# Optimization experiments

Measured on AMD Instinct MI355X. Metric: run time of the kernel, lower is better.

Reference implementation:

```python
import jax, jax.numpy as jnp
import numpy as np

N_ATOMS = 20
N_IN, N_EMB_N, N_EMB_E, N_H_N, N_H_E = 4, 128, 128, 256, 256


def lstm_seq(x, Wi, bi, Wh, bh):
    """x: [B, M, T, D] -> h sequence [B, M, T, H]. Gates stacked as (i,f,g,o).
    Equivalent to the per-gate nn.Linear pairs: bi/bh are the two bias vectors."""
    B, M, T, D = x.shape
    H = Wh.shape[0]
    # precompute all input-to-hidden projections in one big GEMM: [T,B,M,4H]
    xg = jnp.einsum('bmtd,dg->tbmg', x, Wi) + bi

    def step(carry, xg_t):
        c, h = carry
        g = xg_t + h @ Wh + bh  # [B,M,4H]
        i, f, gg, o = jnp.split(g, 4, axis=-1)
        i = jax.nn.sigmoid(i)
        f = jax.nn.sigmoid(f)
        gg = jnp.tanh(gg)
        o = jax.nn.sigmoid(o)
        c = f * c + i * gg
        h = o * jnp.tanh(c)
        return (c, h), h

    z = jnp.zeros((B, M, H), x.dtype)
    _, hs = jax.lax.scan(step, (z, z), xg)  # hs: [T,B,M,H]
    return jnp.transpose(hs, (1, 2, 0, 3))


def setup_inputs() -> dict:
    key = jax.random.key(0)
    ks = jax.random.split(key, 16)
    s = 0.05
    # fully-connected directed edges without self loops -> one-hot incidence
    send, rec = np.where(~np.eye(N_ATOMS, dtype=bool))
    eye = np.eye(N_ATOMS, dtype=np.float32)
    inp = {
        'X': jax.random.normal(ks[0], (16, N_ATOMS, 64, N_IN), jnp.float32),
        'rel_rec': jnp.asarray(eye[rec]),
        'rel_send': jnp.asarray(eye[send]),
        # motion embedding fc
        'Wm': jax.random.normal(ks[1], (N_IN, N_EMB_N), jnp.float32) * s,
        'bm': jnp.zeros((N_EMB_N,), jnp.float32),
        # motion LSTM (gates i,f,g,o stacked)
        'Wmi': jax.random.normal(ks[2], (N_EMB_N, 4 * N_H_N), jnp.float32) * s,
        'bmi': jnp.zeros((4 * N_H_N,), jnp.float32),
        'Wmh': jax.random.normal(ks[3], (N_H_N, 4 * N_H_N), jnp.float32) * s,
        'bmh': jnp.zeros((4 * N_H_N,), jnp.float32),
        # interaction embedding fc (in = 2*n_h_node)
        'We': jax.random.normal(ks[4], (2 * N_H_N, N_EMB_E), jnp.float32) * s,
        'be': jnp.zeros((N_EMB_E,), jnp.float32),
        # edge LSTM
        'Wei': jax.random.normal(ks[5], (N_EMB_E, 4 * N_H_E), jnp.float32) * s,
        'bei': jnp.zeros((4 * N_H_E,), jnp.float32),
        'Weh': jax.random.normal(ks[6], (N_H_E, 4 * N_H_E), jnp.float32) * s,
        'beh': jnp.zeros((4 * N_H_E,), jnp.float32),
        # output fc
        'Wf': jax.random.normal(ks[7], (N_H_E, 1), jnp.float32) * s,
        'bf': jnp.zeros((1,), jnp.float32),
    }
    return inp


def reference(X, rel_rec, rel_send, Wm, bm, Wmi, bmi, Wmh, bmh,
              We, be, Wei, bei, Weh, beh, Wf, bf):
    # Motion embedding on temporal deltas: [B,N,T-1,n_emb_node]
    dX = X[:, :, 1:, :] - X[:, :, :-1, :]
    em = dX @ Wm + bm
    # Motion LSTM, full sequence: [B,N,T-1,Hn]
    hm = lstm_seq(em, Wmi, bmi, Wmh, bmh)
    # Interaction embedding: gather per-edge sender/receiver node states
    senders = jnp.einsum('en,bnth->beth', rel_send, hm)
    receivers = jnp.einsum('en,bnth->beth', rel_rec, hm)
    edges = jnp.concatenate([senders, receivers], axis=-1)  # [B,E,T-1,2Hn]
    ea = edges @ We + be  # [B,E,T-1,n_emb_edge]
    # Edge LSTM, last hidden state: [B,E,He]
    he = lstm_seq(ea, Wei, bei, Weh, beh)[:, :, -1, :]
    # Edge scores -> dense adjacency via incidence matrices
    A = jax.nn.sigmoid(he @ Wf + bf)[..., 0]  # [B,E]
    Ad = jnp.einsum('en,be,em->bnm', rel_send, A, rel_rec)  # send^T diag(A) rec
    return 0.5 * (Ad + jnp.transpose(Ad, (0, 2, 1)))  # symmetrize
```

## Files before the change

kernel.cpp:

```cpp
#include <hip/hip_runtime.h>
#include <stdint.h>

#define NBATCH 16
#define NNODE  20
#define TSTEPS 63
#define NEDGE  380
#define HID    256
#define RS     280

typedef __bf16 bf16x8 __attribute__((ext_vector_type(8)));
typedef float  f32x4  __attribute__((ext_vector_type(4)));

__device__ __forceinline__ float bf2f(unsigned short u){
  union { unsigned int i; float f; } v; v.i = ((unsigned int)u) << 16; return v.f;
}
__device__ __forceinline__ unsigned short f2bf(float f){
  union { float f; unsigned int i; } v; v.f = f;
  return (unsigned short)((v.i + 0x7FFFu + ((v.i >> 16) & 1u)) >> 16);
}
__device__ __forceinline__ bf16x8 as_frag(uint4 v){
  union { uint4 u; bf16x8 b; } c; c.u = v; return c.b;
}
__device__ __forceinline__ float sigmf(float x){ return 1.0f/(1.0f+__expf(-x)); }
__device__ __forceinline__ float tanh_f(float x){ float e=__expf(2.0f*x); return (e-1.0f)/(e+1.0f); }

__device__ __forceinline__ unsigned long long load_ax(const unsigned long long* p){
  return __hip_atomic_load(p, __ATOMIC_RELAXED, __HIP_MEMORY_SCOPE_AGENT);
}
__device__ __forceinline__ void store_ax(unsigned long long* p, unsigned long long v){
  __hip_atomic_store(p, v, __ATOMIC_RELAXED, __HIP_MEMORY_SCOPE_AGENT);
}
__device__ __forceinline__ void wait_vm0(){ asm volatile("s_waitcnt vmcnt(0)" ::: "memory"); }

__device__ __forceinline__ void xpose4(f32x4& v, int cl){
  float s0 = __shfl_xor((float)v[1], 1), s1 = __shfl_xor((float)v[0], 1);
  float s2 = __shfl_xor((float)v[3], 1), s3 = __shfl_xor((float)v[2], 1);
  bool b0 = (cl & 1);
  float a0 = b0 ? s0 : v[0], a1 = b0 ? v[1] : s1;
  float a2 = b0 ? s2 : v[2], a3 = b0 ? v[3] : s3;
  float t0 = __shfl_xor(a2, 2), t1 = __shfl_xor(a3, 2);
  float t2 = __shfl_xor(a0, 2), t3 = __shfl_xor(a1, 2);
  bool b1 = (cl & 2);
  v[0] = b1 ? t0 : a0; v[1] = b1 ? t1 : a1;
  v[2] = b1 ? a2 : t2; v[3] = b1 ? a3 : t3;
}

__global__ __launch_bounds__(256) void prep_a(
    const float* __restrict__ We, const float* __restrict__ Wei,
    const float* __restrict__ Wm, const float* __restrict__ Wmi,
    const float* __restrict__ bm, const float* __restrict__ bmi, const float* __restrict__ bmh,
    const float* __restrict__ be, const float* __restrict__ bei, const float* __restrict__ beh,
    float* __restrict__ Wse, float* __restrict__ Wre, float* __restrict__ WcmGI,
    float* __restrict__ bcmGI, float* __restrict__ bceGI,
    float* __restrict__ Afin, unsigned int* __restrict__ ectr, unsigned int* __restrict__ mctr){
  int bid = blockIdx.x, tid = threadIdx.x;
  if (bid < 2048){
    int idx = bid*256 + tid;
    int half = idx >> 18;
    int j = idx & 262143;
    int k = j >> 10, nn = j & 1023;
    const float* Wrow = We + (half*256 + k)*128;
    float s = 0.f;
    for (int d = 0; d < 128; ++d) s += Wrow[d] * Wei[d*1024 + nn];
    (half ? Wre : Wse)[k*1024 + nn] = s;
  } else if (bid < 2064){
    int idx = (bid-2048)*256 + tid;
    int d = idx >> 10, ci = idx & 1023;
    int col = (ci & 3)*256 + (ci >> 2);
    float s = 0.f;
    for (int j = 0; j < 128; ++j) s += Wm[d*128 + j] * Wmi[j*1024 + col];
    WcmGI[idx] = s;
  } else if (bid < 2068){
    int ci = (bid-2064)*256 + tid;
    int col = (ci & 3)*256 + (ci >> 2);
    float s = bmi[col] + bmh[col];
    for (int j = 0; j < 128; ++j) s += bm[j] * Wmi[j*1024 + col];
    bcmGI[ci] = s;
  } else if (bid < 2072){
    int ci = (bid-2068)*256 + tid;
    int col = (ci & 3)*256 + (ci >> 2);
    float s = bei[col] + beh[col];
    for (int j = 0; j < 128; ++j) s += be[j] * Wei[j*1024 + col];
    bceGI[ci] = s;
  } else if (bid == 2072){
    for (int i = tid; i < 2048; i += 256) ectr[i] = 0u;
    for (int i = tid; i < 1024; i += 256) mctr[i] = 0u;
  } else {
    int idx = (bid-2073)*256 + tid;
    if (idx < NBATCH*NEDGE) Afin[idx] = 0.f;
  }
}

__device__ __forceinline__ void pack_gi(const float* __restrict__ W,
                                        unsigned short* __restrict__ dst, int id){
  int lane = id & 63, kt = (id >> 6) & 7, tt = (id >> 9) & 1, w = (id >> 10) & 7, nb = id >> 13;
  int cl = lane & 15, q = lane >> 4;
  int gcol = (cl & 3)*256 + nb*64 + (w*2 + tt)*4 + (cl >> 2);
  int k0 = kt*32 + q*8;
  unsigned int wb[4];
  #pragma unroll
  for (int p = 0; p < 4; ++p){
    unsigned short a = f2bf(W[(k0+2*p  )*1024 + gcol]);
    unsigned short b = f2bf(W[(k0+2*p+1)*1024 + gcol]);
    wb[p] = (unsigned int)a | ((unsigned int)b << 16);
  }
  ((uint4*)dst)[id] = make_uint4(wb[0], wb[1], wb[2], wb[3]);
}

__device__ __forceinline__ void pack_one(const float* __restrict__ S,
                                         unsigned short* __restrict__ dst, int id, int n){
  int lane = id & 63, kt = (id >> 6) & 7;
  int k0 = kt*32 + ((lane >> 4) << 3);
  unsigned int wb[4];
  #pragma unroll
  for (int p = 0; p < 4; ++p){
    unsigned short a = f2bf(S[(k0+2*p  )*1024 + n]);
    unsigned short b = f2bf(S[(k0+2*p+1)*1024 + n]);
    wb[p] = (unsigned int)a | ((unsigned int)b << 16);
  }
  ((uint4*)dst)[id] = make_uint4(wb[0], wb[1], wb[2], wb[3]);
}

__global__ __launch_bounds__(256) void prep_b(
    const float* __restrict__ Wmh, const float* __restrict__ Weh,
    const float* __restrict__ Wse, const float* __restrict__ Wre,
    unsigned short* __restrict__ pWmh, unsigned short* __restrict__ pWeh,
    unsigned short* __restrict__ pWsr){
  int gid = blockIdx.x*256 + threadIdx.x;
  if (gid < 32768){
    pack_gi(Wmh, pWmh, gid);
  } else if (gid < 65536){
    pack_gi(Weh, pWeh, gid - 32768);
  } else {
    int id = gid - 65536;
    int ng = (id >> 9)*16 + (id & 15);
    const float* S = (ng < 1024) ? Wse : Wre;
    pack_one(S, pWsr, id, ng & 1023);
  }
}

__global__ __launch_bounds__(512, 2) void motion_lstm(
    const float* __restrict__ X, const float* __restrict__ WcmGI,
    const float* __restrict__ bcmGI, const unsigned short* __restrict__ pWmh,
    unsigned short* __restrict__ hm, unsigned short* __restrict__ mb,
    unsigned int* __restrict__ mctr){
  __shared__ __align__(16) unsigned short hst[16*RS];
  __shared__ float dxs[10*252];
  __shared__ __align__(16) float sWc[4*256];
  __shared__ __align__(16) float sbc[256];
  int tid = threadIdx.x, lane = tid & 63, w = tid >> 6;
  int l15 = lane & 15, quad = lane >> 4;
  int m = blockIdx.x & 31, n = blockIdx.x >> 5;
  int s0 = m*10;
  unsigned int* ctr = mctr + m*32;

  uint4 wreg[2][8];
  #pragma unroll
  for (int tt = 0; tt < 2; ++tt)
    #pragma unroll
    for (int kt = 0; kt < 8; ++kt)
      wreg[tt][kt] = ((const uint4*)pWmh)[(((n*8 + w)*2 + tt)*8 + kt)*64 + lane];

  uint4 z4 = make_uint4(0,0,0,0);
  for (int i = tid; i < 560; i += 512) ((uint4*)hst)[i] = z4;
  for (int i = tid; i < 1024; i += 512) sWc[i] = WcmGI[(i >> 8)*1024 + n*256 + (i & 255)];
  if (tid < 256) sbc[tid] = bcmGI[n*256 + tid];
  for (int i = tid; i < 2520; i += 512){
    int sl = i / 252; int r = i % 252; int t = r >> 2; int d = r & 3;
    const float* Xp = X + (((size_t)(s0 + sl)*64 + t)*4 + d);
    dxs[i] = Xp[4] - Xp[0];
  }
  __syncthreads();

  float bb[2] = { sbc[(w*2+0)*16 + l15], sbc[(w*2+1)*16 + l15] };
  int row = quad*4 + (l15 & 3);
  int hsub = l15 >> 2;
  int slr = row < 10 ? row : 9;
  float ce[2] = {0.f, 0.f};

  for (int t = 0; t < TSTEPS; ++t){
    if (t > 0){
      if (tid == 0){
        unsigned int tgt = 4u*(unsigned)t;
        while (__hip_atomic_load(ctr, __ATOMIC_RELAXED, __HIP_MEMORY_SCOPE_AGENT) < tgt)
          __builtin_amdgcn_s_sleep(1);
      }
      __syncthreads();
      const unsigned long long* mbp = (const unsigned long long*)mb
          + ((size_t)((t-1)&1)*32 + m)*16*64;
      unsigned long long pv[2]; int po[2] = {-1,-1};
      #pragma unroll
      for (int j = 0; j < 2; ++j){
        int i = tid + j*512;
        if (i < 768){
          int which = i >> 8, jj = i & 255;
          int r = jj >> 4, c = jj & 15;
          int np = which + (which >= n ? 1 : 0);
          pv[j] = load_ax(&mbp[(size_t)r*64 + np*16 + c]);
          po[j] = r*RS + np*64 + c*4;
        }
      }
      #pragma unroll
      for (int j = 0; j < 2; ++j)
        if (po[j] >= 0) *(unsigned long long*)&hst[po[j]] = pv[j];
    }
    __syncthreads();

    f32x4 acc[2];
    acc[0] = (f32x4){bb[0],bb[0],bb[0],bb[0]};
    acc[1] = (f32x4){bb[1],bb[1],bb[1],bb[1]};
    #pragma unroll
    for (int kt = 0; kt < 8; ++kt){
      bf16x8 a = as_frag(*(const uint4*)&hst[l15*RS + kt*32 + quad*8]);
      acc[0] = __builtin_amdgcn_mfma_f32_16x16x32_bf16(a, as_frag(wreg[0][kt]), acc[0], 0, 0, 0);
      acc[1] = __builtin_amdgcn_mfma_f32_16x16x32_bf16(a, as_frag(wreg[1][kt]), acc[1], 0, 0, 0);
    }
    __syncthreads();

    f32x4 dxv = *(const f32x4*)&dxs[slr*252 + t*4];
    #pragma unroll
    for (int tt = 0; tt < 2; ++tt){
      int tl = w*2 + tt;
      f32x4 v = acc[tt];
      xpose4(v, l15);
      #pragma unroll
      for (int d = 0; d < 4; ++d){
        f32x4 wv = *(const f32x4*)&sWc[d*256 + tl*16 + hsub*4];
        v[0] += dxv[d]*wv[0]; v[1] += dxv[d]*wv[1];
        v[2] += dxv[d]*wv[2]; v[3] += dxv[d]*wv[3];
      }
      float iv = sigmf(v[0]), fv = sigmf(v[1]), gg = tanh_f(v[2]), ov = sigmf(v[3]);
      float cc = fv*ce[tt] + iv*gg; ce[tt] = cc;
      hst[row*RS + n*64 + tl*4 + hsub] = f2bf(ov*tanh_f(cc));
    }
    __syncthreads();

    unsigned long long* mbc = (unsigned long long*)mb
        + ((size_t)(t&1)*32 + m)*16*64;
    if (tid < 256){
      int r = tid >> 4, c = tid & 15;
      unsigned long long v = *(const unsigned long long*)&hst[r*RS + n*64 + c*4];
      if (t < 62) store_ax(&mbc[(size_t)r*64 + n*16 + c], v);
      if (r < 10){
        int seq = s0 + r;
        int b2 = seq / 20, nd = seq - (seq/20)*20;
        *(unsigned long long*)&hm[(((size_t)(b2*63 + t)*20) + nd)*256 + n*64 + c*4] = v;
      }
    }
    wait_vm0();
    __syncthreads();
    if (t < 62 && tid == 0)
      __hip_atomic_fetch_add(ctr, 1u, __ATOMIC_RELAXED, __HIP_MEMORY_SCOPE_AGENT);
  }
}

__global__ __launch_bounds__(256) void gsr_gemm(
    const unsigned short* __restrict__ hm, const unsigned short* __restrict__ pWsr,
    unsigned short* __restrict__ gsrT){
  __shared__ __align__(16) unsigned short scol[128*100];
  int tid = threadIdx.x, lane = tid & 63, wid = tid >> 6;
  int l15 = lane & 15, quad = lane >> 4;
  int bm = blockIdx.x % 252, bn = blockIdx.x / 252;
  int rowbase = bm*80;
  f32x4 acc[5][2] = {};
  #pragma unroll
  for (int kt = 0; kt < 8; ++kt){
    bf16x8 af[5];
    #pragma unroll
    for (int mt = 0; mt < 5; ++mt)
      af[mt] = as_frag(*(const uint4*)&hm[(size_t)(rowbase + mt*16 + l15)*256 + kt*32 + quad*8]);
    #pragma unroll
    for (int j = 0; j < 2; ++j){
      int ntg = bn*8 + wid*2 + j;
      bf16x8 bfr = as_frag(*(const uint4*)&pWsr[(((size_t)ntg*8 + kt)*64 + lane)*8]);
      #pragma unroll
      for (int mt = 0; mt < 5; ++mt)
        acc[mt][j] = __builtin_amdgcn_mfma_f32_16x16x32_bf16(af[mt], bfr, acc[mt][j], 0, 0, 0);
    }
  }
  #pragma unroll
  for (int mt = 0; mt < 5; ++mt)
    #pragma unroll
    for (int j = 0; j < 2; ++j){
      int colL = (wid*2 + j)*16 + l15;
      unsigned int p0 = (unsigned)f2bf(acc[mt][j][0]) | ((unsigned)f2bf(acc[mt][j][1]) << 16);
      unsigned int p1 = (unsigned)f2bf(acc[mt][j][2]) | ((unsigned)f2bf(acc[mt][j][3]) << 16);
      *(uint2*)&scol[colL*100 + mt*16 + quad*4] = make_uint2(p0, p1);
    }
  __syncthreads();
  int half = bn >> 3;
  #pragma unroll
  for (int rep = 0; rep < 2; ++rep){
    int i = tid + rep*256;
    int btl = i >> 7, colL = i & 127;
    const unsigned short* sp = &scol[colL*100 + btl*20];
    uint2 u0 = *(const uint2*)(sp);
    uint2 u1 = *(const uint2*)(sp+4);
    uint2 u2 = *(const uint2*)(sp+8);
    uint2 u3 = *(const uint2*)(sp+12);
    uint2 u4 = *(const uint2*)(sp+16);
    unsigned short* dp = gsrT + ((size_t)(bm*4 + btl)*1024 + (bn&7)*128 + colL)*48;
    if (half){
      *(uint4*)(dp)      = make_uint4(u0.x, u0.y, u1.x, u1.y);
      *(uint4*)(dp + 8)  = make_uint4(u2.x, u2.y, u3.x, u3.y);
      *(uint2*)(dp + 16) = u4;
    } else {
      unsigned int o0 = u0.x, o1 = u0.y, o2 = u1.x & 0xffffu;
      unsigned int o3 = (u1.x >> 16) | (u1.y << 16);
      unsigned int o4 = (u1.y >> 16) | (u2.x << 16);
      unsigned int o5 = u2.x >> 16;
      unsigned int o6 = u2.y, o7 = u3.x, o8 = u3.y & 0xffffu;
      unsigned int o9 = (u3.y >> 16) | (u4.x << 16);
      unsigned int o10 = (u4.x >> 16) | (u4.y << 16);
      unsigned int o11 = u4.y >> 16;
      *(uint4*)(dp + 24) = make_uint4(o0, o1, o2, o3);
      *(uint4*)(dp + 32) = make_uint4(o4, o5, o6, o7);
      *(uint4*)(dp + 40) = make_uint4(o8, o9, o10, o11);
    }
  }
}

__device__ __forceinline__ void stage_gxb(const unsigned short* __restrict__ gsrT,
                                          unsigned short* __restrict__ gx,
                                          int tid, int b, int m, int n, int tq){
  const unsigned short* base = gsrT + (size_t)(b*63 + tq)*1024*48;
  int c = tid >> 1, chv = tid & 1;
  int g = c >> 6, hh = c & 63;
  const unsigned short* src = base + (size_t)((g << 8) + (n << 6) + hh)*48;
  unsigned short* dst = gx + (hh >> 2)*640 + (((hh & 3) << 2) + g)*40;
  if (chv == 0){
    *(uint4*)(dst)      = *(const uint4*)(src);
    *(uint4*)(dst + 8)  = *(const uint4*)(src + 8);
    *(uint2*)(dst + 16) = *(const uint2*)(src + 16);
  } else {
    const unsigned int* s3 = (const unsigned int*)(src + 24 + 6*m);
    unsigned int* d3 = (unsigned int*)(dst + 24);
    d3[0] = s3[0]; d3[1] = s3[1]; d3[2] = s3[2];
  }
}

__global__ __launch_bounds__(512, 2) void edge_lstm(
    const unsigned short* __restrict__ gsrT, const float* __restrict__ bceGI,
    const unsigned short* __restrict__ pWeh, const float* __restrict__ Wf,
    unsigned short* __restrict__ hb, float* __restrict__ Afin,
    unsigned int* __restrict__ ectr){
  __shared__ __align__(16) unsigned short hst[96*RS];
  __shared__ __align__(16) unsigned short gxb[2][10240];
  __shared__ __align__(16) float sbce[256];
  __shared__ __align__(16) float sWf[64];
  int tid = threadIdx.x, lane = tid & 63, w = tid >> 6;
  int l15 = lane & 15, quad = lane >> 4;
  int bid = blockIdx.x;
  int n = bid >> 6, G = bid & 63, b = G >> 2, m = G & 3;
  int e0 = m*95;
  unsigned int* ctr = ectr + G*32;

  uint4 wreg[2][8];
  #pragma unroll
  for (int tt = 0; tt < 2; ++tt)
    #pragma unroll
    for (int kt = 0; kt < 8; ++kt)
      wreg[tt][kt] = ((const uint4*)pWeh)[(((n*8 + w)*2 + tt)*8 + kt)*64 + lane];

  uint4 aoh[6];
  #pragma unroll
  for (int mt = 0; mt < 6; ++mt){
    int row = mt*16 + l15;
    int e = e0 + (row < 95 ? row : 94);
    int s = e / 19; int rr = e - s*19;
    int sr = s - m*5;
    int rc = rr + (rr >= s ? 1 : 0);
    unsigned int wd[4];
    #pragma unroll
    for (int p = 0; p < 4; ++p){
      int k0 = quad*8 + 2*p, k1 = k0 + 1;
      unsigned short a0 = ((k0 < 20) ? (rc == k0) : (k0 >= 24 && k0 < 29 && sr == k0-24)) ? 0x3F80 : 0;
      unsigned short a1 = ((k1 < 20) ? (rc == k1) : (k1 >= 24 && k1 < 29 && sr == k1-24)) ? 0x3F80 : 0;
      wd[p] = (unsigned int)a0 | ((unsigned int)a1 << 16);
    }
    aoh[mt] = make_uint4(wd[0], wd[1], wd[2], wd[3]);
  }

  if (tid < 256) sbce[tid] = bceGI[n*256 + tid];
  if (tid < 64)  sWf[tid]  = Wf[n*64 + tid];
  uint4 z4 = make_uint4(0,0,0,0);
  for (int i = tid; i < 3360; i += 512) ((uint4*)hst)[i] = z4;
  for (int i = tid; i < 2560; i += 512) ((uint4*)gxb)[i] = z4;
  __syncthreads();
  stage_gxb(gsrT, &gxb[0][0], tid, b, m, n, 0);
  __syncthreads();

  float bb[2]  = { sbce[(w*2+0)*16 + l15], sbce[(w*2+1)*16 + l15] };
  float wfr[2] = { sWf[(w*2+0)*4 + (l15>>2)], sWf[(w*2+1)*4 + (l15>>2)] };

  float ce[2][6]; float epi[6];
  #pragma unroll
  for (int mt = 0; mt < 6; ++mt){ ce[0][mt] = 0.f; ce[1][mt] = 0.f; epi[mt] = 0.f; }

  for (int t = 0; t < TSTEPS; ++t){
    int par = t & 1, nxt = par ^ 1;
    if (t > 0){
      if (tid == 0){
        unsigned int tgt = 4u*(unsigned)t;
        while (__hip_atomic_load(ctr, __ATOMIC_RELAXED, __HIP_MEMORY_SCOPE_AGENT) < tgt)
          __builtin_amdgcn_s_sleep(1);
      }
      __syncthreads();
      const unsigned long long* hbp = (const unsigned long long*)hb
          + (((size_t)((t-1)&1)*16 + b)*4 + m)*96*64;
      unsigned long long pv[9]; int po[9];
      #pragma unroll
      for (int j = 0; j < 9; ++j){
        int i = tid + j*512;
        int which = i / 1536, jj = i - which*1536;
        int r = jj >> 4, c = jj & 15;
        int np = which + (which >= n ? 1 : 0);
        pv[j] = load_ax(&hbp[(size_t)r*64 + np*16 + c]);
        po[j] = r*RS + np*64 + c*4;
      }
      #pragma unroll
      for (int j = 0; j < 9; ++j)
        *(unsigned long long*)&hst[po[j]] = pv[j];
    }
    if (t + 1 < TSTEPS)
      stage_gxb(gsrT, &gxb[nxt][0], tid, b, m, n, t+1);
    __syncthreads();

    f32x4 acc[2][6];
    #pragma unroll
    for (int mt = 0; mt < 6; ++mt){
      acc[0][mt] = (f32x4){bb[0],bb[0],bb[0],bb[0]};
      acc[1][mt] = (f32x4){bb[1],bb[1],bb[1],bb[1]};
    }
    #pragma unroll
    for (int kt = 0; kt < 8; ++kt){
      bf16x8 a[6];
      #pragma unroll
      for (int mt = 0; mt < 6; ++mt)
        a[mt] = as_frag(*(const uint4*)&hst[(mt*16 + l15)*RS + kt*32 + quad*8]);
      #pragma unroll
      for (int mt = 0; mt < 6; ++mt){
        acc[0][mt] = __builtin_amdgcn_mfma_f32_16x16x32_bf16(a[mt], as_frag(wreg[0][kt]), acc[0][mt], 0, 0, 0);
        acc[1][mt] = __builtin_amdgcn_mfma_f32_16x16x32_bf16(a[mt], as_frag(wreg[1][kt]), acc[1][mt], 0, 0, 0);
      }
    }
    {
      bf16x8 bx0 = as_frag(*(const uint4*)&gxb[par][(w*2+0)*640 + l15*40 + quad*8]);
      bf16x8 bx1 = as_frag(*(const uint4*)&gxb[par][(w*2+1)*640 + l15*40 + quad*8]);
      #pragma unroll
      for (int mt = 0; mt < 6; ++mt){
        acc[0][mt] = __builtin_amdgcn_mfma_f32_16x16x32_bf16(as_frag(aoh[mt]), bx0, acc[0][mt], 0, 0, 0);
        acc[1][mt] = __builtin_amdgcn_mfma_f32_16x16x32_bf16(as_frag(aoh[mt]), bx1, acc[1][mt], 0, 0, 0);
      }
    }
    __syncthreads();

    #pragma unroll
    for (int tt = 0; tt < 2; ++tt){
      int tl = w*2 + tt;
      #pragma unroll
      for (int mt = 0; mt < 6; ++mt){
        f32x4 v = acc[tt][mt];
        xpose4(v, l15);
        float iv = sigmf(v[0]), fv = sigmf(v[1]), gg = tanh_f(v[2]), ov = sigmf(v[3]);
        float cc = fv*ce[tt][mt] + iv*gg; ce[tt][mt] = cc;
        float h = ov*tanh_f(cc);
        if (t < 62){
          int row = mt*16 + quad*4 + (l15 & 3);
          hst[row*RS + n*64 + tl*4 + (l15>>2)] = f2bf(h);
        } else {
          epi[mt] += h * wfr[tt];
        }
      }
    }
    if (t < 62){
      __syncthreads();
      unsigned long long* hbc = (unsigned long long*)hb
          + (((size_t)(t&1)*16 + b)*4 + m)*96*64;
      #pragma unroll
      for (int j = 0; j < 3; ++j){
        int i = tid + j*512;
        int r = i >> 4, c = i & 15;
        unsigned long long v = *(const unsigned long long*)&hst[r*RS + n*64 + c*4];
        store_ax(&hbc[(size_t)r*64 + n*16 + c], v);
      }
      wait_vm0();
      __syncthreads();
      if (tid == 0)
        __hip_atomic_fetch_add(ctr, 1u, __ATOMIC_RELAXED, __HIP_MEMORY_SCOPE_AGENT);
    }
  }
  #pragma unroll
  for (int mt = 0; mt < 6; ++mt){
    float v = epi[mt];
    v += __shfl_xor(v, 4);
    v += __shfl_xor(v, 8);
    if (l15 < 4){
      int row = mt*16 + quad*4 + l15;
      if (row < 95)
        atomicAdd(&Afin[b*380 + e0 + row], v);
    }
  }
}

__global__ __launch_bounds__(256) void finalize(const float* __restrict__ Afin,
                                                const float* __restrict__ bfp,
                                                float* __restrict__ out){
  int idx = blockIdx.x*256 + threadIdx.x;
  if (idx >= 16*400) return;
  int b = idx / 400; int ij = idx % 400; int i = ij / 20; int j = ij % 20;
  float v = 0.f;
  if (i != j){
    int e1 = i*19 + j - (j > i ? 1 : 0);
    int e2 = j*19 + i - (i > j ? 1 : 0);
    float bf = bfp[0];
    v = 0.5f*(sigmf(Afin[b*380 + e1] + bf) + sigmf(Afin[b*380 + e2] + bf));
  }
  out[idx] = v;
}

extern "C" void kernel_launch(void* const* d_in, const int* in_sizes, int n_in,
                              void* d_out, int out_size, void* d_ws, size_t ws_size,
                              hipStream_t stream){
  (void)in_sizes; (void)n_in; (void)out_size; (void)ws_size;
  const float* X   = (const float*)d_in[0];
  const float* Wm  = (const float*)d_in[3];
  const float* bm  = (const float*)d_in[4];
  const float* Wmi = (const float*)d_in[5];
  const float* bmi = (const float*)d_in[6];
  const float* Wmh = (const float*)d_in[7];
  const float* bmh = (const float*)d_in[8];
  const float* We  = (const float*)d_in[9];
  const float* be  = (const float*)d_in[10];
  const float* Wei = (const float*)d_in[11];
  const float* bei = (const float*)d_in[12];
  const float* Weh = (const float*)d_in[13];
  const float* beh = (const float*)d_in[14];
  const float* Wf  = (const float*)d_in[15];
  const float* bfp = (const float*)d_in[16];

  char* ws = (char*)d_ws;
  float* Wse   = (float*)(ws + 0);
  float* Wre   = (float*)(ws + 1048576);
  float* WcmGI = (float*)(ws + 2097152);
  float* bcmGI = (float*)(ws + 2113536);
  float* bceGI = (float*)(ws + 2117632);
  unsigned short* pWmh = (unsigned short*)(ws + 2121728);
  unsigned short* pWeh = (unsigned short*)(ws + 2646016);
  unsigned short* pWsr = (unsigned short*)(ws + 3170304);
  unsigned short* hm   = (unsigned short*)(ws + 4218880);
  unsigned short* gsrT = (unsigned short*)(ws + 14540800);
  unsigned short* hb   = (unsigned short*)(ws + 113631232);
  unsigned short* mb   = hb;
  float* Afin          = (float*)(ws + 119922688);
  unsigned int* ectr   = (unsigned int*)(ws + 119947264);
  unsigned int* mctr   = (unsigned int*)(ws + 119955456);
  float* out = (float*)d_out;

  hipLaunchKernelGGL(prep_a, dim3(2097), dim3(256), 0, stream,
                     We, Wei, Wm, Wmi, bm, bmi, bmh, be, bei, beh,
                     Wse, Wre, WcmGI, bcmGI, bceGI, Afin, ectr, mctr);
  hipLaunchKernelGGL(prep_b, dim3(512), dim3(256), 0, stream,
                     Wmh, Weh, Wse, Wre, pWmh, pWeh, pWsr);
  {
    void* margs[] = {(void*)&X, (void*)&WcmGI, (void*)&bcmGI, (void*)&pWmh,
                     (void*)&hm, (void*)&mb, (void*)&mctr};
    hipLaunchCooperativeKernel(reinterpret_cast<void*>(motion_lstm),
                               dim3(128), dim3(512), margs, 0, stream);
  }
  hipLaunchKernelGGL(gsr_gemm, dim3(252*16), dim3(256), 0, stream,
                     hm, pWsr, gsrT);
  {
    void* eargs[] = {(void*)&gsrT, (void*)&bceGI, (void*)&pWeh, (void*)&Wf,
                     (void*)&hb, (void*)&Afin, (void*)&ectr};
    hipLaunchCooperativeKernel(reinterpret_cast<void*>(edge_lstm),
                               dim3(256), dim3(512), eargs, 0, stream);
  }
  hipLaunchKernelGGL(finalize, dim3(25), dim3(256), 0, stream,
                     Afin, bfp, out);
}
```

Measured before the change: 1.055 ms.

## Split edge LSTM over 512 blocks with 48-edge row groups

Re-partitions the cooperative edge LSTM from 256 blocks of 95 edges each to 512 blocks of 48 edges each. The gsr layout now stores the sender projection for every sender, so a block can read four sender rows at an arbitrary offset. Shared hidden-state staging, counters and MFMA tiles shrink to match, and launch bounds rise to allow more blocks per CU. This spreads the serial recurrence across more CUs to cut per-step latency, at the cost of more inter-block synchronisation traffic and partly wasted tiles.

```diff
diff --git a/kernel.cpp b/kernel.cpp
--- a/kernel.cpp
+++ b/kernel.cpp
@@ -83,7 +83,7 @@
     for (int j = 0; j < 128; ++j) s += be[j] * Wei[j*1024 + col];
     bceGI[ci] = s;
   } else if (bid == 2072){
-    for (int i = tid; i < 2048; i += 256) ectr[i] = 0u;
+    for (int i = tid; i < 4096; i += 256) ectr[i] = 0u;
     for (int i = tid; i < 1024; i += 256) mctr[i] = 0u;
   } else {
     int idx = (bid-2073)*256 + tid;
@@ -288,7 +288,8 @@
       *(uint2*)&scol[colL*100 + mt*16 + quad*4] = make_uint2(p0, p1);
     }
   __syncthreads();
-  int half = bn >> 3;
+  int recv = bn >> 3;
+  int doff = recv ? 0 : 24;
   #pragma unroll
   for (int rep = 0; rep < 2; ++rep){
     int i = tid + rep*256;
@@ -299,30 +300,16 @@
     uint2 u2 = *(const uint2*)(sp+8);
     uint2 u3 = *(const uint2*)(sp+12);
     uint2 u4 = *(const uint2*)(sp+16);
-    unsigned short* dp = gsrT + ((size_t)(bm*4 + btl)*1024 + (bn&7)*128 + colL)*48;
-    if (half){
-      *(uint4*)(dp)      = make_uint4(u0.x, u0.y, u1.x, u1.y);
-      *(uint4*)(dp + 8)  = make_uint4(u2.x, u2.y, u3.x, u3.y);
-      *(uint2*)(dp + 16) = u4;
-    } else {
-      unsigned int o0 = u0.x, o1 = u0.y, o2 = u1.x & 0xffffu;
-      unsigned int o3 = (u1.x >> 16) | (u1.y << 16);
-      unsigned int o4 = (u1.y >> 16) | (u2.x << 16);
-      unsigned int o5 = u2.x >> 16;
-      unsigned int o6 = u2.y, o7 = u3.x, o8 = u3.y & 0xffffu;
-      unsigned int o9 = (u3.y >> 16) | (u4.x << 16);
-      unsigned int o10 = (u4.x >> 16) | (u4.y << 16);
-      unsigned int o11 = u4.y >> 16;
-      *(uint4*)(dp + 24) = make_uint4(o0, o1, o2, o3);
-      *(uint4*)(dp + 32) = make_uint4(o4, o5, o6, o7);
-      *(uint4*)(dp + 40) = make_uint4(o8, o9, o10, o11);
-    }
+    unsigned short* dp = gsrT + ((size_t)(bm*4 + btl)*1024 + (bn&7)*128 + colL)*48 + doff;
+    *(uint4*)(dp)      = make_uint4(u0.x, u0.y, u1.x, u1.y);
+    *(uint4*)(dp + 8)  = make_uint4(u2.x, u2.y, u3.x, u3.y);
+    *(uint2*)(dp + 16) = u4;
   }
 }
 
 __device__ __forceinline__ void stage_gxb(const unsigned short* __restrict__ gsrT,
                                           unsigned short* __restrict__ gx,
-                                          int tid, int b, int m, int n, int tq){
+                                          int tid, int b, int smin, int n, int tq){
   const unsigned short* base = gsrT + (size_t)(b*63 + tq)*1024*48;
   int c = tid >> 1, chv = tid & 1;
   int g = c >> 6, hh = c & 63;
@@ -333,26 +320,27 @@
     *(uint4*)(dst + 8)  = *(const uint4*)(src + 8);
     *(uint2*)(dst + 16) = *(const uint2*)(src + 16);
   } else {
-    const unsigned int* s3 = (const unsigned int*)(src + 24 + 6*m);
-    unsigned int* d3 = (unsigned int*)(dst + 24);
-    d3[0] = s3[0]; d3[1] = s3[1]; d3[2] = s3[2];
-  }
-}
-
-__global__ __launch_bounds__(512, 2) void edge_lstm(
+    const unsigned short* s3 = src + 24 + smin;
+    dst[24] = s3[0]; dst[25] = s3[1]; dst[26] = s3[2]; dst[27] = s3[3];
+  }
+}
+
+__global__ __launch_bounds__(512, 4) void edge_lstm(
     const unsigned short* __restrict__ gsrT, const float* __restrict__ bceGI,
     const unsigned short* __restrict__ pWeh, const float* __restrict__ Wf,
     unsigned short* __restrict__ hb, float* __restrict__ Afin,
     unsigned int* __restrict__ ectr){
-  __shared__ __align__(16) unsigned short hst[96*RS];
+  __shared__ __align__(16) unsigned short hst[48*RS];
   __shared__ __align__(16) unsigned short gxb[2][10240];
   __shared__ __align__(16) float sbce[256];
   __shared__ __align__(16) float sWf[64];
   int tid = threadIdx.x, lane = tid & 63, w = tid >> 6;
   int l15 = lane & 15, quad = lane >> 4;
   int bid = blockIdx.x;
-  int n = bid >> 6, G = bid & 63, b = G >> 2, m = G & 3;
-  int e0 = m*95;
+  int n = bid >> 7, G = bid & 127, b = G >> 3, m = G & 7;
+  int e0 = m*48;
+  int valid = NEDGE - e0 < 48 ? NEDGE - e0 : 48;
+  int smin = e0 / 19;
   unsigned int* ctr = ectr + G*32;
 
   uint4 wreg[2][8];
@@ -362,20 +350,20 @@
     for (int kt = 0; kt < 8; ++kt)
       wreg[tt][kt] = ((const uint4*)pWeh)[(((n*8 + w)*2 + tt)*8 + kt)*64 + lane];
 
-  uint4 aoh[6];
-  #pragma unroll
-  for (int mt = 0; mt < 6; ++mt){
+  uint4 aoh[3];
+  #pragma unroll
+  for (int mt = 0; mt < 3; ++mt){
     int row = mt*16 + l15;
-    int e = e0 + (row < 95 ? row : 94);
+    int e = e0 + (row < valid ? row : valid-1);
     int s = e / 19; int rr = e - s*19;
-    int sr = s - m*5;
+    int sr = s - smin;
     int rc = rr + (rr >= s ? 1 : 0);
     unsigned int wd[4];
     #pragma unroll
     for (int p = 0; p < 4; ++p){
       int k0 = quad*8 + 2*p, k1 = k0 + 1;
-      unsigned short a0 = ((k0 < 20) ? (rc == k0) : (k0 >= 24 && k0 < 29 && sr == k0-24)) ? 0x3F80 : 0;
-      unsigned short a1 = ((k1 < 20) ? (rc == k1) : (k1 >= 24 && k1 < 29 && sr == k1-24)) ? 0x3F80 : 0;
+      unsigned short a0 = ((k0 < 20) ? (rc == k0) : (k0 >= 24 && k0 < 28 && sr == k0-24)) ? 0x3F80 : 0;
+      unsigned short a1 = ((k1 < 20) ? (rc == k1) : (k1 >= 24 && k1 < 28 && sr == k1-24)) ? 0x3F80 : 0;
       wd[p] = (unsigned int)a0 | ((unsigned int)a1 << 16);
     }
     aoh[mt] = make_uint4(wd[0], wd[1], wd[2], wd[3]);
@@ -384,18 +372,18 @@
   if (tid < 256) sbce[tid] = bceGI[n*256 + tid];
   if (tid < 64)  sWf[tid]  = Wf[n*64 + tid];
   uint4 z4 = make_uint4(0,0,0,0);
-  for (int i = tid; i < 3360; i += 512) ((uint4*)hst)[i] = z4;
+  for (int i = tid; i < 1680; i += 512) ((uint4*)hst)[i] = z4;
   for (int i = tid; i < 2560; i += 512) ((uint4*)gxb)[i] = z4;
   __syncthreads();
-  stage_gxb(gsrT, &gxb[0][0], tid, b, m, n, 0);
+  stage_gxb(gsrT, &gxb[0][0], tid, b, smin, n, 0);
   __syncthreads();
 
   float bb[2]  = { sbce[(w*2+0)*16 + l15], sbce[(w*2+1)*16 + l15] };
   float wfr[2] = { sWf[(w*2+0)*4 + (l15>>2)], sWf[(w*2+1)*4 + (l15>>2)] };
 
-  float ce[2][6]; float epi[6];
-  #pragma unroll
-  for (int mt = 0; mt < 6; ++mt){ ce[0][mt] = 0.f; ce[1][mt] = 0.f; epi[mt] = 0.f; }
+  float ce[2][3]; float epi[3];
+  #pragma unroll
+  for (int mt = 0; mt < 3; ++mt){ ce[0][mt] = 0.f; ce[1][mt] = 0.f; epi[mt] = 0.f; }
 
   for (int t = 0; t < TSTEPS; ++t){
     int par = t & 1, nxt = par ^ 1;
@@ -407,39 +395,41 @@
       }
       __syncthreads();
       const unsigned long long* hbp = (const unsigned long long*)hb
-          + (((size_t)((t-1)&1)*16 + b)*4 + m)*96*64;
-      unsigned long long pv[9]; int po[9];
-      #pragma unroll
-      for (int j = 0; j < 9; ++j){
+          + (((size_t)((t-1)&1)*16 + b)*8 + m)*48*64;
+      unsigned long long pv[5]; int po[5] = {-1,-1,-1,-1,-1};
+      #pragma unroll
+      for (int j = 0; j < 5; ++j){
         int i = tid + j*512;
-        int which = i / 1536, jj = i - which*1536;
-        int r = jj >> 4, c = jj & 15;
-        int np = which + (which >= n ? 1 : 0);
-        pv[j] = load_ax(&hbp[(size_t)r*64 + np*16 + c]);
-        po[j] = r*RS + np*64 + c*4;
-      }
-      #pragma unroll
-      for (int j = 0; j < 9; ++j)
-        *(unsigned long long*)&hst[po[j]] = pv[j];
+        if (i < 2304){
+          int which = i / 768, jj = i - which*768;
+          int r = jj >> 4, c = jj & 15;
+          int np = which + (which >= n ? 1 : 0);
+          pv[j] = load_ax(&hbp[(size_t)r*64 + np*16 + c]);
+          po[j] = r*RS + np*64 + c*4;
+        }
+      }
+      #pragma unroll
+      for (int j = 0; j < 5; ++j)
+        if (po[j] >= 0) *(unsigned long long*)&hst[po[j]] = pv[j];
     }
     if (t + 1 < TSTEPS)
-      stage_gxb(gsrT, &gxb[nxt][0], tid, b, m, n, t+1);
+      stage_gxb(gsrT, &gxb[nxt][0], tid, b, smin, n, t+1);
     __syncthreads();
 
-    f32x4 acc[2][6];
-    #pragma unroll
-    for (int mt = 0; mt < 6; ++mt){
+    f32x4 acc[2][3];
+    #pragma unroll
+    for (int mt = 0; mt < 3; ++mt){
       acc[0][mt] = (f32x4){bb[0],bb[0],bb[0],bb[0]};
       acc[1][mt] = (f32x4){bb[1],bb[1],bb[1],bb[1]};
     }
     #pragma unroll
     for (int kt = 0; kt < 8; ++kt){
-      bf16x8 a[6];
-      #pragma unroll
-      for (int mt = 0; mt < 6; ++mt)
+      bf16x8 a[3];
+      #pragma unroll
+      for (int mt = 0; mt < 3; ++mt)
         a[mt] = as_frag(*(const uint4*)&hst[(mt*16 + l15)*RS + kt*32 + quad*8]);
       #pragma unroll
-      for (int mt = 0; mt < 6; ++mt){
+      for (int mt = 0; mt < 3; ++mt){
         acc[0][mt] = __builtin_amdgcn_mfma_f32_16x16x32_bf16(a[mt], as_frag(wreg[0][kt]), acc[0][mt], 0, 0, 0);
         acc[1][mt] = __builtin_amdgcn_mfma_f32_16x16x32_bf16(a[mt], as_frag(wreg[1][kt]), acc[1][mt], 0, 0, 0);
       }
@@ -448,7 +438,7 @@
       bf16x8 bx0 = as_frag(*(const uint4*)&gxb[par][(w*2+0)*640 + l15*40 + quad*8]);
       bf16x8 bx1 = as_frag(*(const uint4*)&gxb[par][(w*2+1)*640 + l15*40 + quad*8]);
       #pragma unroll
-      for (int mt = 0; mt < 6; ++mt){
+      for (int mt = 0; mt < 3; ++mt){
         acc[0][mt] = __builtin_amdgcn_mfma_f32_16x16x32_bf16(as_frag(aoh[mt]), bx0, acc[0][mt], 0, 0, 0);
         acc[1][mt] = __builtin_amdgcn_mfma_f32_16x16x32_bf16(as_frag(aoh[mt]), bx1, acc[1][mt], 0, 0, 0);
       }
@@ -459,7 +449,7 @@
     for (int tt = 0; tt < 2; ++tt){
       int tl = w*2 + tt;
       #pragma unroll
-      for (int mt = 0; mt < 6; ++mt){
+      for (int mt = 0; mt < 3; ++mt){
         f32x4 v = acc[tt][mt];
         xpose4(v, l15);
         float iv = sigmf(v[0]), fv = sigmf(v[1]), gg = tanh_f(v[2]), ov = sigmf(v[3]);
@@ -476,13 +466,15 @@
     if (t < 62){
       __syncthreads();
       unsigned long long* hbc = (unsigned long long*)hb
-          + (((size_t)(t&1)*16 + b)*4 + m)*96*64;
-      #pragma unroll
-      for (int j = 0; j < 3; ++j){
+          + (((size_t)(t&1)*16 + b)*8 + m)*48*64;
+      #pragma unroll
+      for (int j = 0; j < 2; ++j){
         int i = tid + j*512;
-        int r = i >> 4, c = i & 15;
-        unsigned long long v = *(const unsigned long long*)&hst[r*RS + n*64 + c*4];
-        store_ax(&hbc[(size_t)r*64 + n*16 + c], v);
+        if (i < 768){
+          int r = i >> 4, c = i & 15;
+          unsigned long long v = *(const unsigned long long*)&hst[r*RS + n*64 + c*4];
+          store_ax(&hbc[(size_t)r*64 + n*16 + c], v);
+        }
       }
       wait_vm0();
       __syncthreads();
@@ -491,13 +483,13 @@
     }
   }
   #pragma unroll
-  for (int mt = 0; mt < 6; ++mt){
+  for (int mt = 0; mt < 3; ++mt){
     float v = epi[mt];
     v += __shfl_xor(v, 4);
     v += __shfl_xor(v, 8);
     if (l15 < 4){
       int row = mt*16 + quad*4 + l15;
-      if (row < 95)
+      if (row < valid)
         atomicAdd(&Afin[b*380 + e0 + row], v);
     }
   }
@@ -554,7 +546,7 @@
   unsigned short* mb   = hb;
   float* Afin          = (float*)(ws + 119922688);
   unsigned int* ectr   = (unsigned int*)(ws + 119947264);
-  unsigned int* mctr   = (unsigned int*)(ws + 119955456);
+  unsigned int* mctr   = (unsigned int*)(ws + 119963648);
   float* out = (float*)d_out;
 
   hipLaunchKernelGGL(prep_a, dim3(2097), dim3(256), 0, stream,
@@ -574,7 +566,7 @@
     void* eargs[] = {(void*)&gsrT, (void*)&bceGI, (void*)&pWeh, (void*)&Wf,
                      (void*)&hb, (void*)&Afin, (void*)&ectr};
     hipLaunchCooperativeKernel(reinterpret_cast<void*>(edge_lstm),
-                               dim3(256), dim3(512), eargs, 0, stream);
+                               dim3(512), dim3(512), eargs, 0, stream);
   }
   hipLaunchKernelGGL(finalize, dim3(25), dim3(256), 0, stream,
                      Afin, bfp, out);
```

Measured after the change: 1.510 ms. +43.1%, slower.

## Double-buffer LSTM hidden state and publish h directly from registers

Applied to the files above, without the earlier changes.

Both recurrent LSTM kernels now keep two hidden-state buffers in shared memory. Each step's new h is written to the next buffer and packed across lanes with shuffles so it can be stored straight to the global exchange buffer and hm. This removes two __syncthreads and the shared-memory read-back pass per timestep. The gsr_gemm output layout is also simplified so both halves use the same contiguous store path, and the staging reads adjust to match. Spin-waits gain an iteration cap, and the counter regions are enlarged and moved.

```diff
diff --git a/kernel.cpp b/kernel.cpp
--- a/kernel.cpp
+++ b/kernel.cpp
@@ -7,6 +7,7 @@
 #define NEDGE  380
 #define HID    256
 #define RS     280
+#define SPIN_MAX (1u << 23)
 
 typedef __bf16 bf16x8 __attribute__((ext_vector_type(8)));
 typedef float  f32x4  __attribute__((ext_vector_type(4)));
@@ -31,6 +32,14 @@
   __hip_atomic_store(p, v, __ATOMIC_RELAXED, __HIP_MEMORY_SCOPE_AGENT);
 }
 __device__ __forceinline__ void wait_vm0(){ asm volatile("s_waitcnt vmcnt(0)" ::: "memory"); }
+
+__device__ __forceinline__ void spin_until(const unsigned int* ctr, unsigned int tgt){
+  unsigned int guard = 0;
+  while (__hip_atomic_load(ctr, __ATOMIC_RELAXED, __HIP_MEMORY_SCOPE_AGENT) < tgt){
+    if (++guard > SPIN_MAX) break;
+    __builtin_amdgcn_s_sleep(1);
+  }
+}
 
 __device__ __forceinline__ void xpose4(f32x4& v, int cl){
   float s0 = __shfl_xor((float)v[1], 1), s1 = __shfl_xor((float)v[0], 1);
@@ -43,6 +52,14 @@
   bool b1 = (cl & 2);
   v[0] = b1 ? t0 : a0; v[1] = b1 ? t1 : a1;
   v[2] = b1 ? a2 : t2; v[3] = b1 ? a3 : t3;
+}
+
+__device__ __forceinline__ unsigned long long pack_h4(unsigned int hv, int l15){
+  unsigned int o4 = (unsigned int)__shfl_xor((int)hv, 4);
+  unsigned int lo = ((l15 & 4) == 0) ? ((hv & 0xffffu) | (o4 << 16))
+                                     : ((o4 & 0xffffu) | (hv << 16));
+  unsigned int hi = (unsigned int)__shfl_xor((int)lo, 8);
+  return ((unsigned long long)hi << 32) | (unsigned long long)lo;
 }
 
 __global__ __launch_bounds__(256) void prep_a(
@@ -83,7 +100,7 @@
     for (int j = 0; j < 128; ++j) s += be[j] * Wei[j*1024 + col];
     bceGI[ci] = s;
   } else if (bid == 2072){
-    for (int i = tid; i < 2048; i += 256) ectr[i] = 0u;
+    for (int i = tid; i < 4096; i += 256) ectr[i] = 0u;
     for (int i = tid; i < 1024; i += 256) mctr[i] = 0u;
   } else {
     int idx = (bid-2073)*256 + tid;
@@ -144,7 +161,7 @@
     const float* __restrict__ bcmGI, const unsigned short* __restrict__ pWmh,
     unsigned short* __restrict__ hm, unsigned short* __restrict__ mb,
     unsigned int* __restrict__ mctr){
-  __shared__ __align__(16) unsigned short hst[16*RS];
+  __shared__ __align__(16) unsigned short hst[2][16*RS];
   __shared__ float dxs[10*252];
   __shared__ __align__(16) float sWc[4*256];
   __shared__ __align__(16) float sbc[256];
@@ -162,7 +179,7 @@
       wreg[tt][kt] = ((const uint4*)pWmh)[(((n*8 + w)*2 + tt)*8 + kt)*64 + lane];
 
   uint4 z4 = make_uint4(0,0,0,0);
-  for (int i = tid; i < 560; i += 512) ((uint4*)hst)[i] = z4;
+  for (int i = tid; i < 1120; i += 512) ((uint4*)hst)[i] = z4;
   for (int i = tid; i < 1024; i += 512) sWc[i] = WcmGI[(i >> 8)*1024 + n*256 + (i & 255)];
   if (tid < 256) sbc[tid] = bcmGI[n*256 + tid];
   for (int i = tid; i < 2520; i += 512){
@@ -179,12 +196,9 @@
   float ce[2] = {0.f, 0.f};
 
   for (int t = 0; t < TSTEPS; ++t){
+    int par = t & 1, nxt = par ^ 1;
     if (t > 0){
-      if (tid == 0){
-        unsigned int tgt = 4u*(unsigned)t;
-        while (__hip_atomic_load(ctr, __ATOMIC_RELAXED, __HIP_MEMORY_SCOPE_AGENT) < tgt)
-          __builtin_amdgcn_s_sleep(1);
-      }
+      if (tid == 0) spin_until(ctr, 4u*(unsigned)t);
       __syncthreads();
       const unsigned long long* mbp = (const unsigned long long*)mb
           + ((size_t)((t-1)&1)*32 + m)*16*64;
@@ -202,7 +216,7 @@
       }
       #pragma unroll
       for (int j = 0; j < 2; ++j)
-        if (po[j] >= 0) *(unsigned long long*)&hst[po[j]] = pv[j];
+        if (po[j] >= 0) *(unsigned long long*)&hst[par][po[j]] = pv[j];
     }
     __syncthreads();
 
@@ -211,12 +225,13 @@
     acc[1] = (f32x4){bb[1],bb[1],bb[1],bb[1]};
     #pragma unroll
     for (int kt = 0; kt < 8; ++kt){
-      bf16x8 a = as_frag(*(const uint4*)&hst[l15*RS + kt*32 + quad*8]);
+      bf16x8 a = as_frag(*(const uint4*)&hst[par][l15*RS + kt*32 + quad*8]);
       acc[0] = __builtin_amdgcn_mfma_f32_16x16x32_bf16(a, as_frag(wreg[0][kt]), acc[0], 0, 0, 0);
       acc[1] = __builtin_amdgcn_mfma_f32_16x16x32_bf16(a, as_frag(wreg[1][kt]), acc[1], 0, 0, 0);
     }
-    __syncthreads();
-
+
+    unsigned long long* mbc = (unsigned long long*)mb
+        + ((size_t)(t&1)*32 + m)*16*64;
     f32x4 dxv = *(const f32x4*)&dxs[slr*252 + t*4];
     #pragma unroll
     for (int tt = 0; tt < 2; ++tt){
@@ -231,26 +246,25 @@
       }
       float iv = sigmf(v[0]), fv = sigmf(v[1]), gg = tanh_f(v[2]), ov = sigmf(v[3]);
       float cc = fv*ce[tt] + iv*gg; ce[tt] = cc;
-      hst[row*RS + n*64 + tl*4 + hsub] = f2bf(ov*tanh_f(cc));
-    }
-    __syncthreads();
-
-    unsigned long long* mbc = (unsigned long long*)mb
-        + ((size_t)(t&1)*32 + m)*16*64;
-    if (tid < 256){
-      int r = tid >> 4, c = tid & 15;
-      unsigned long long v = *(const unsigned long long*)&hst[r*RS + n*64 + c*4];
-      if (t < 62) store_ax(&mbc[(size_t)r*64 + n*16 + c], v);
-      if (r < 10){
-        int seq = s0 + r;
-        int b2 = seq / 20, nd = seq - (seq/20)*20;
-        *(unsigned long long*)&hm[(((size_t)(b2*63 + t)*20) + nd)*256 + n*64 + c*4] = v;
-      }
-    }
-    wait_vm0();
-    __syncthreads();
-    if (t < 62 && tid == 0)
-      __hip_atomic_fetch_add(ctr, 1u, __ATOMIC_RELAXED, __HIP_MEMORY_SCOPE_AGENT);
+      unsigned short hb16 = f2bf(ov*tanh_f(cc));
+      if (t < 62) hst[nxt][row*RS + n*64 + tl*4 + hsub] = hb16;
+      unsigned long long uv = pack_h4((unsigned int)hb16, l15);
+      if ((l15 & 12) == 0){
+        int r = quad*4 + l15;
+        if (t < 62) store_ax(&mbc[(size_t)r*64 + n*16 + w*2 + tt], uv);
+        if (r < 10){
+          int seq = s0 + r;
+          int b2 = seq / 20, nd = seq - b2*20;
+          *(unsigned long long*)&hm[(((size_t)(b2*63 + t)*20) + nd)*256 + n*64 + tl*4] = uv;
+        }
+      }
+    }
+    if (t < 62){
+      wait_vm0();
+      __syncthreads();
+      if (tid == 0)
+        __hip_atomic_fetch_add(ctr, 1u, __ATOMIC_RELAXED, __HIP_MEMORY_SCOPE_AGENT);
+    }
   }
 }
 
@@ -288,7 +302,8 @@
       *(uint2*)&scol[colL*100 + mt*16 + quad*4] = make_uint2(p0, p1);
     }
   __syncthreads();
-  int half = bn >> 3;
+  int recv = bn >> 3;
+  int doff = recv ? 0 : 24;
   #pragma unroll
   for (int rep = 0; rep < 2; ++rep){
     int i = tid + rep*256;
@@ -299,30 +314,16 @@
     uint2 u2 = *(const uint2*)(sp+8);
     uint2 u3 = *(const uint2*)(sp+12);
     uint2 u4 = *(const uint2*)(sp+16);
-    unsigned short* dp = gsrT + ((size_t)(bm*4 + btl)*1024 + (bn&7)*128 + colL)*48;
-    if (half){
-      *(uint4*)(dp)      = make_uint4(u0.x, u0.y, u1.x, u1.y);
-      *(uint4*)(dp + 8)  = make_uint4(u2.x, u2.y, u3.x, u3.y);
-      *(uint2*)(dp + 16) = u4;
-    } else {
-      unsigned int o0 = u0.x, o1 = u0.y, o2 = u1.x & 0xffffu;
-      unsigned int o3 = (u1.x >> 16) | (u1.y << 16);
-      unsigned int o4 = (u1.y >> 16) | (u2.x << 16);
-      unsigned int o5 = u2.x >> 16;
-      unsigned int o6 = u2.y, o7 = u3.x, o8 = u3.y & 0xffffu;
-      unsigned int o9 = (u3.y >> 16) | (u4.x << 16);
-      unsigned int o10 = (u4.x >> 16) | (u4.y << 16);
-      unsigned int o11 = u4.y >> 16;
-      *(uint4*)(dp + 24) = make_uint4(o0, o1, o2, o3);
-      *(uint4*)(dp + 32) = make_uint4(o4, o5, o6, o7);
-      *(uint4*)(dp + 40) = make_uint4(o8, o9, o10, o11);
-    }
+    unsigned short* dp = gsrT + ((size_t)(bm*4 + btl)*1024 + (bn&7)*128 + colL)*48 + doff;
+    *(uint4*)(dp)      = make_uint4(u0.x, u0.y, u1.x, u1.y);
+    *(uint4*)(dp + 8)  = make_uint4(u2.x, u2.y, u3.x, u3.y);
+    *(uint2*)(dp + 16) = u4;
   }
 }
 
 __device__ __forceinline__ void stage_gxb(const unsigned short* __restrict__ gsrT,
                                           unsigned short* __restrict__ gx,
-                                          int tid, int b, int m, int n, int tq){
+                                          int tid, int b, int smin, int n, int tq){
   const unsigned short* base = gsrT + (size_t)(b*63 + tq)*1024*48;
   int c = tid >> 1, chv = tid & 1;
   int g = c >> 6, hh = c & 63;
@@ -333,9 +334,8 @@
     *(uint4*)(dst + 8)  = *(const uint4*)(src + 8);
     *(uint2*)(dst + 16) = *(const uint2*)(src + 16);
   } else {
-    const unsigned int* s3 = (const unsigned int*)(src + 24 + 6*m);
-    unsigned int* d3 = (unsigned int*)(dst + 24);
-    d3[0] = s3[0]; d3[1] = s3[1]; d3[2] = s3[2];
+    const unsigned short* s3 = src + 24 + smin;
+    dst[24]=s3[0]; dst[25]=s3[1]; dst[26]=s3[2]; dst[27]=s3[3]; dst[28]=s3[4];
   }
 }
 
@@ -344,7 +344,7 @@
     const unsigned short* __restrict__ pWeh, const float* __restrict__ Wf,
     unsigned short* __restrict__ hb, float* __restrict__ Afin,
     unsigned int* __restrict__ ectr){
-  __shared__ __align__(16) unsigned short hst[96*RS];
+  __shared__ __align__(16) unsigned short hst[2][96*RS];
   __shared__ __align__(16) unsigned short gxb[2][10240];
   __shared__ __align__(16) float sbce[256];
   __shared__ __align__(16) float sWf[64];
@@ -384,10 +384,10 @@
   if (tid < 256) sbce[tid] = bceGI[n*256 + tid];
   if (tid < 64)  sWf[tid]  = Wf[n*64 + tid];
   uint4 z4 = make_uint4(0,0,0,0);
-  for (int i = tid; i < 3360; i += 512) ((uint4*)hst)[i] = z4;
+  for (int i = tid; i < 6720; i += 512) ((uint4*)hst)[i] = z4;
   for (int i = tid; i < 2560; i += 512) ((uint4*)gxb)[i] = z4;
   __syncthreads();
-  stage_gxb(gsrT, &gxb[0][0], tid, b, m, n, 0);
+  stage_gxb(gsrT, &gxb[0][0], tid, b, m*5, n, 0);
   __syncthreads();
 
   float bb[2]  = { sbce[(w*2+0)*16 + l15], sbce[(w*2+1)*16 + l15] };
@@ -400,11 +400,7 @@
   for (int t = 0; t < TSTEPS; ++t){
     int par = t & 1, nxt = par ^ 1;
     if (t > 0){
-      if (tid == 0){
-        unsigned int tgt = 4u*(unsigned)t;
-        while (__hip_atomic_load(ctr, __ATOMIC_RELAXED, __HIP_MEMORY_SCOPE_AGENT) < tgt)
-          __builtin_amdgcn_s_sleep(1);
-      }
+      if (tid == 0) spin_until(ctr, 4u*(unsigned)t);
       __syncthreads();
       const unsigned long long* hbp = (const unsigned long long*)hb
           + (((size_t)((t-1)&1)*16 + b)*4 + m)*96*64;
@@ -420,10 +416,10 @@
       }
       #pragma unroll
       for (int j = 0; j < 9; ++j)
-        *(unsigned long long*)&hst[po[j]] = pv[j];
+        *(unsigned long long*)&hst[par][po[j]] = pv[j];
     }
     if (t + 1 < TSTEPS)
-      stage_gxb(gsrT, &gxb[nxt][0], tid, b, m, n, t+1);
+      stage_gxb(gsrT, &gxb[nxt][0], tid, b, m*5, n, t+1);
     __syncthreads();
 
     f32x4 acc[2][6];
@@ -437,7 +433,7 @@
       bf16x8 a[6];
       #pragma unroll
       for (int mt = 0; mt < 6; ++mt)
-        a[mt] = as_frag(*(const uint4*)&hst[(mt*16 + l15)*RS + kt*32 + quad*8]);
+        a[mt] = as_frag(*(const uint4*)&hst[par][(mt*16 + l15)*RS + kt*32 + quad*8]);
       #pragma unroll
       for (int mt = 0; mt < 6; ++mt){
         acc[0][mt] = __builtin_amdgcn_mfma_f32_16x16x32_bf16(a[mt], as_frag(wreg[0][kt]), acc[0][mt], 0, 0, 0);
@@ -453,8 +449,9 @@
         acc[1][mt] = __builtin_amdgcn_mfma_f32_16x16x32_bf16(as_frag(aoh[mt]), bx1, acc[1][mt], 0, 0, 0);
       }
     }
-    __syncthreads();
-
+
+    unsigned long long* hbc = (unsigned long long*)hb
+        + (((size_t)(t&1)*16 + b)*4 + m)*96*64;
     #pragma unroll
     for (int tt = 0; tt < 2; ++tt){
       int tl = w*2 + tt;
@@ -466,24 +463,18 @@
         float cc = fv*ce[tt][mt] + iv*gg; ce[tt][mt] = cc;
         float h = ov*tanh_f(cc);
         if (t < 62){
-          int row = mt*16 + quad*4 + (l15 & 3);
-          hst[row*RS + n*64 + tl*4 + (l15>>2)] = f2bf(h);
+          unsigned short hb16 = f2bf(h);
+          int row2 = mt*16 + quad*4 + (l15 & 3);
+          hst[nxt][row2*RS + n*64 + tl*4 + (l15>>2)] = hb16;
+          unsigned long long uv = pack_h4((unsigned int)hb16, l15);
+          if ((l15 & 12) == 0)
+            store_ax(&hbc[(size_t)(mt*16 + quad*4 + l15)*64 + n*16 + tl], uv);
         } else {
           epi[mt] += h * wfr[tt];
         }
       }
     }
     if (t < 62){
-      __syncthreads();
-      unsigned long long* hbc = (unsigned long long*)hb
-          + (((size_t)(t&1)*16 + b)*4 + m)*96*64;
-      #pragma unroll
-      for (int j = 0; j < 3; ++j){
-        int i = tid + j*512;
-        int r = i >> 4, c = i & 15;
-        unsigned long long v = *(const unsigned long long*)&hst[r*RS + n*64 + c*4];
-        store_ax(&hbc[(size_t)r*64 + n*16 + c], v);
-      }
       wait_vm0();
       __syncthreads();
       if (tid == 0)
@@ -554,7 +545,7 @@
   unsigned short* mb   = hb;
   float* Afin          = (float*)(ws + 119922688);
   unsigned int* ectr   = (unsigned int*)(ws + 119947264);
-  unsigned int* mctr   = (unsigned int*)(ws + 119955456);
+  unsigned int* mctr   = (unsigned int*)(ws + 119963648);
   float* out = (float*)d_out;
 
   hipLaunchKernelGGL(prep_a, dim3(2097), dim3(256), 0, stream,
```

New measurement: 1.078 ms. 2.1% more time.
